# Kernel tuning notes

Hardware: AMD Instinct MI355X
Metric: run time of the kernel (lower is better)

## Reference

```python
import jax, jax.numpy as jnp
import numpy as np

N, C, S = 16, 512, 4096

def setup_inputs() -> dict:
    rng = jax.random.key(0)
    k1, k2, k3 = jax.random.split(rng, 3)
    return {
        "key": jax.random.normal(k1, (N, C, S), dtype=jnp.float32),
        "value": jax.random.normal(k2, (N, C, S), dtype=jnp.float32),
        "query": jax.random.normal(k3, (N, C, S), dtype=jnp.float32),
    }

def reference(key, value, query):
    KC = key.shape[1]
    # query.permute(0,2,1): [N, C, S] -> [N, S, C]
    # sim_map = bmm(key, query^T): [N, C, C], scaled by KC^-0.5
    sim = jnp.einsum("ncs,nds->ncd", key, query) * (KC ** -0.5)
    # softmax over dim=1 (first C axis)
    sim = jax.nn.softmax(sim, axis=1)
    # context = bmm(sim, value): [N, C, C] @ [N, C, S] -> [N, C, S]
    context = jnp.einsum("ncd,nds->ncs", sim, value)
    return context
```

## Files before the change

kernel.cpp:

```cpp
#include <hip/hip_runtime.h>

typedef __bf16 bf16x8 __attribute__((ext_vector_type(8)));
typedef float f32x4 __attribute__((ext_vector_type(4)));
typedef unsigned short u16;
typedef u16 u16x4 __attribute__((ext_vector_type(4)));
typedef u16 u16x8 __attribute__((ext_vector_type(8)));

__device__ __forceinline__ u16 f2bf(float f) {
  unsigned u = __builtin_bit_cast(unsigned, f);
  unsigned r = (u + 0x7fffu + ((u >> 16) & 1u)) >> 16;
  return (u16)r;
}

__device__ __forceinline__ void gld_lds16(const u16* g, u16* l) {
  __builtin_amdgcn_global_load_lds(
      (__attribute__((address_space(1))) void*)(g),
      (__attribute__((address_space(3))) void*)(l), 16, 0, 0);
}

__device__ __forceinline__ f32x4 ntload4(const float* p) {
  return __builtin_nontemporal_load((const f32x4*)p);
}

__global__ __launch_bounds__(256) void k_cvt(const float* __restrict__ K,
                                             const float* __restrict__ Q,
                                             u16* __restrict__ Kb,
                                             u16* __restrict__ Qb) {
  const float* src = blockIdx.y ? Q : K;
  u16* dst = blockIdx.y ? Qb : Kb;
  const size_t i = (size_t)blockIdx.x * 2048 + threadIdx.x * 8;
  f32x4 a = ntload4(src + i);
  f32x4 b = ntload4(src + i + 4);
  u16x8 h;
  h[0] = f2bf(a[0]); h[1] = f2bf(a[1]); h[2] = f2bf(a[2]); h[3] = f2bf(a[3]);
  h[4] = f2bf(b[0]); h[5] = f2bf(b[1]); h[6] = f2bf(b[2]); h[7] = f2bf(b[3]);
  *(u16x8*)(dst + i) = h;
}

__global__ __launch_bounds__(512) void k_mix(const u16* __restrict__ Kb,
                                             const u16* __restrict__ Qb,
                                             float* __restrict__ Lp,
                                             const float* __restrict__ V,
                                             u16* __restrict__ Vt) {
  extern __shared__ char raw[];
  const int bid = blockIdx.x;
  const int t = threadIdx.x;

  if (bid % 5 == 0) {
    u16* sA = (u16*)raw;
    u16* sB = (u16*)(raw + 32768);
    const int sid0 = bid / 5;
    const int sid = (sid0 & 7) * 64 + (sid0 >> 3);
    const int n = sid >> 5;
    const int rem = sid & 31;
    const int kc = rem >> 4;
    const int r2 = rem & 15;
    const int cy = r2 >> 2, dx = r2 & 3;
    const int lane = t & 63, wid = t >> 6;
    const int wr = wid >> 2, wc = wid & 3;
    const float scale = 0.04419417382415922f;

    const u16* Ab = Kb + ((size_t)n * 512 + cy * 128) * 4096 + kc * 2048;
    const u16* Bb = Qb + ((size_t)n * 512 + dx * 128) * 4096 + kc * 2048;
    f32x4 acc[4][2] = {};
    const int srow0 = t >> 3;
    const int scol = ((t & 7) << 3) ^ ((srow0 & 7) << 3);

#define MIX_STAGE(buf, k0)                                                      \
  {                                                                             \
    _Pragma("unroll") for (int q = 0; q < 2; ++q) {                             \
      const int row = q * 64 + srow0;                                           \
      gld_lds16(Ab + (size_t)row * 4096 + (k0) + scol,                          \
                sA + (buf) * 8192 + (q * 512 + (wid << 6)) * 8);                \
      gld_lds16(Bb + (size_t)row * 4096 + (k0) + scol,                          \
                sB + (buf) * 8192 + (q * 512 + (wid << 6)) * 8);                \
    }                                                                           \
  }
#define MIX_COMPUTE(buf)                                                        \
  {                                                                             \
    _Pragma("unroll") for (int ki = 0; ki < 2; ++ki) {                          \
      bf16x8 a[4], b[2];                                                        \
      const int ce = ki * 32 + (lane >> 4) * 8;                                 \
      _Pragma("unroll") for (int mi = 0; mi < 4; ++mi) {                        \
        const int r = wr * 64 + mi * 16 + (lane & 15);                          \
        a[mi] = *(const bf16x8*)&sA[(buf) * 8192 + r * 64 + (ce ^ ((r & 7) << 3))]; \
      }                                                                         \
      _Pragma("unroll") for (int ni = 0; ni < 2; ++ni) {                        \
        const int r = wc * 32 + ni * 16 + (lane & 15);                          \
        b[ni] = *(const bf16x8*)&sB[(buf) * 8192 + r * 64 + (ce ^ ((r & 7) << 3))]; \
      }                                                                         \
      __builtin_amdgcn_s_setprio(1);                                            \
      _Pragma("unroll") for (int mi = 0; mi < 4; ++mi)                          \
        _Pragma("unroll") for (int ni = 0; ni < 2; ++ni)                        \
          acc[mi][ni] = __builtin_amdgcn_mfma_f32_16x16x32_bf16(                \
              a[mi], b[ni], acc[mi][ni], 0, 0, 0);                              \
      __builtin_amdgcn_s_setprio(0);                                            \
    }                                                                           \
  }

    MIX_STAGE(0, 0);
    __syncthreads();
    int cur = 0;
    for (int kt = 0; kt < 31; ++kt) {
      MIX_STAGE(cur ^ 1, (kt + 1) << 6);
      MIX_COMPUTE(cur);
      __syncthreads();
      cur ^= 1;
    }
    MIX_COMPUTE(cur);

    float* Lb = Lp + ((size_t)kc * 16 + n) * 512 * 512;
    const int c0 = cy * 128, d0 = dx * 128;
#pragma unroll
    for (int mi = 0; mi < 4; ++mi)
#pragma unroll
      for (int ni = 0; ni < 2; ++ni) {
        int colo = d0 + wc * 32 + ni * 16 + (lane & 15);
#pragma unroll
        for (int j = 0; j < 4; ++j) {
          int rowo = c0 + wr * 64 + mi * 16 + ((lane >> 4) << 2) + j;
          Lb[(size_t)rowo * 512 + colo] = acc[mi][ni][j] * scale;
        }
      }
#undef MIX_STAGE
#undef MIX_COMPUTE
  } else {
    const int vid = bid - bid / 5 - 1;
    const int sub = t >> 8, tt = t & 255;
    const int tile = vid * 2 + sub;
    const int n = tile >> 8;
    const int r = tile & 255;
    const int d0 = (r >> 6) * 128, s0 = (r & 63) * 64;
    float* lds = (float*)(raw + sub * 34816);
    {
      const int r0 = tt >> 4, c4 = (tt & 15) << 2;
#pragma unroll
      for (int p = 0; p < 8; ++p) {
        const int dr = r0 + p * 16;
        f32x4 v = ntload4(V + ((size_t)n * 512 + d0 + dr) * 4096 + s0 + c4);
        const int sw = ((dr >> 3) & 7) << 2;
        *(f32x4*)(&lds[dr * 68 + (c4 ^ sw)]) = v;
      }
    }
    __syncthreads();
    {
      const int sr0 = tt >> 4, dcol = (tt & 15) << 3;
#pragma unroll
      for (int p2 = 0; p2 < 4; ++p2) {
        const int sr = sr0 + p2 * 16;
        u16x8 h;
#pragma unroll
        for (int j = 0; j < 8; ++j) {
          const int d = dcol + j;
          h[j] = f2bf(lds[d * 68 + (sr ^ (((d >> 3) & 7) << 2))]);
        }
        *(u16x8*)(Vt + ((size_t)n * 4096 + s0 + sr) * 512 + d0 + dcol) = h;
      }
    }
  }
}

template <int KDIV>
__global__ __launch_bounds__(512) void k_stats2(const float* __restrict__ Lp,
                                                u16* __restrict__ E) {
  __shared__ f32x4 redm[16][32];
  __shared__ f32x4 reds[16][32];
  const int n = blockIdx.y;
  const int tx = threadIdx.x & 31, ty = threadIdx.x >> 5;
  const int d0 = blockIdx.x * 128 + tx * 4;
  const size_t CH = (size_t)16 * 512 * 512;
  const float* B = Lp + (size_t)n * 512 * 512 + d0;

  f32x4 m = {-3.0e38f, -3.0e38f, -3.0e38f, -3.0e38f};
  f32x4 s = {0.f, 0.f, 0.f, 0.f};
  for (int c = ty; c < 512; c += 16) {
    f32x4 v = *(const f32x4*)(B + (size_t)c * 512);
#pragma unroll
    for (int q = 1; q < KDIV; ++q) v += *(const f32x4*)(B + q * CH + (size_t)c * 512);
#pragma unroll
    for (int j = 0; j < 4; ++j) {
      float nm = fmaxf(m[j], v[j]);
      s[j] = s[j] * __expf(m[j] - nm) + __expf(v[j] - nm);
      m[j] = nm;
    }
  }
  redm[ty][tx] = m;
  reds[ty][tx] = s;
  __syncthreads();
  f32x4 M = redm[0][tx], S;
#pragma unroll
  for (int q = 1; q < 16; ++q)
#pragma unroll
    for (int j = 0; j < 4; ++j) M[j] = fmaxf(M[j], redm[q][tx][j]);
#pragma unroll
  for (int j = 0; j < 4; ++j) S[j] = 0.f;
#pragma unroll
  for (int q = 0; q < 16; ++q)
#pragma unroll
    for (int j = 0; j < 4; ++j) S[j] += reds[q][tx][j] * __expf(redm[q][tx][j] - M[j]);
  f32x4 si;
#pragma unroll
  for (int j = 0; j < 4; ++j) si[j] = 1.0f / S[j];

  u16* Eb = E + (size_t)n * 512 * 512 + d0;
  for (int c = ty; c < 512; c += 16) {
    f32x4 v = *(const f32x4*)(B + (size_t)c * 512);
#pragma unroll
    for (int q = 1; q < KDIV; ++q) v += *(const f32x4*)(B + q * CH + (size_t)c * 512);
    u16x4 h;
#pragma unroll
    for (int j = 0; j < 4; ++j) h[j] = f2bf(__expf(v[j] - M[j]) * si[j]);
    *(u16x4*)(Eb + (size_t)c * 512) = h;
  }
}

template <int KDIV>
__global__ __launch_bounds__(512) void k_simk(const u16* __restrict__ Kb,
                                              const u16* __restrict__ Qb,
                                              float* __restrict__ Lp) {
  __shared__ u16 sA[2][128 * 64];
  __shared__ u16 sB[2][128 * 64];
  constexpr int NB = 256 * KDIV;
  const int bid = blockIdx.x;
  const int sid = (bid & 7) * (NB / 8) + (bid >> 3);
  constexpr int PER_N = 16 * KDIV;
  const int n = sid / PER_N;
  const int rem = sid % PER_N;
  const int kc = rem >> 4;
  const int r2 = rem & 15;
  const int cy = r2 >> 2, dx = r2 & 3;
  const int t = threadIdx.x, lane = t & 63, wid = t >> 6;
  const int wr = wid >> 2, wc = wid & 3;
  const float scale = 0.04419417382415922f;

  const u16* Ab = Kb + ((size_t)n * 512 + cy * 128) * 4096 + kc * (4096 / KDIV);
  const u16* Bb = Qb + ((size_t)n * 512 + dx * 128) * 4096 + kc * (4096 / KDIV);
  f32x4 acc[4][2] = {};
  const int srow0 = t >> 3;
  const int scol = ((t & 7) << 3) ^ ((srow0 & 7) << 3);

#define SIM_STAGE(buf, k0)                                                      \
  {                                                                             \
    _Pragma("unroll") for (int q = 0; q < 2; ++q) {                             \
      const int row = q * 64 + srow0;                                           \
      gld_lds16(Ab + (size_t)row * 4096 + (k0) + scol,                          \
                &sA[buf][(q * 512 + (wid << 6)) * 8]);                          \
      gld_lds16(Bb + (size_t)row * 4096 + (k0) + scol,                          \
                &sB[buf][(q * 512 + (wid << 6)) * 8]);                          \
    }                                                                           \
  }
#define SIM_COMPUTE(buf)                                                        \
  {                                                                             \
    _Pragma("unroll") for (int ki = 0; ki < 2; ++ki) {                          \
      bf16x8 a[4], b[2];                                                        \
      const int ce = ki * 32 + (lane >> 4) * 8;                                 \
      _Pragma("unroll") for (int mi = 0; mi < 4; ++mi) {                        \
        const int r = wr * 64 + mi * 16 + (lane & 15);                          \
        a[mi] = *(const bf16x8*)&sA[buf][r * 64 + (ce ^ ((r & 7) << 3))];       \
      }                                                                         \
      _Pragma("unroll") for (int ni = 0; ni < 2; ++ni) {                        \
        const int r = wc * 32 + ni * 16 + (lane & 15);                          \
        b[ni] = *(const bf16x8*)&sB[buf][r * 64 + (ce ^ ((r & 7) << 3))];       \
      }                                                                         \
      _Pragma("unroll") for (int mi = 0; mi < 4; ++mi)                          \
        _Pragma("unroll") for (int ni = 0; ni < 2; ++ni)                        \
          acc[mi][ni] = __builtin_amdgcn_mfma_f32_16x16x32_bf16(                \
              a[mi], b[ni], acc[mi][ni], 0, 0, 0);                              \
    }                                                                           \
  }

  constexpr int NSTEP = 64 / KDIV;
  SIM_STAGE(0, 0);
  __syncthreads();
  int cur = 0;
  for (int kt = 0; kt < NSTEP - 1; ++kt) {
    SIM_STAGE(cur ^ 1, (kt + 1) << 6);
    SIM_COMPUTE(cur);
    __syncthreads();
    cur ^= 1;
  }
  SIM_COMPUTE(cur);

  float* Lb = Lp + ((size_t)kc * 16 + n) * 512 * 512;
  const int c0 = cy * 128, d0 = dx * 128;
#pragma unroll
  for (int mi = 0; mi < 4; ++mi)
#pragma unroll
    for (int ni = 0; ni < 2; ++ni) {
      int colo = d0 + wc * 32 + ni * 16 + (lane & 15);
#pragma unroll
      for (int j = 0; j < 4; ++j) {
        int rowo = c0 + wr * 64 + mi * 16 + ((lane >> 4) << 2) + j;
        Lb[(size_t)rowo * 512 + colo] = acc[mi][ni][j] * scale;
      }
    }
#undef SIM_STAGE
#undef SIM_COMPUTE
}

__global__ __launch_bounds__(256) void k_vt(const float* __restrict__ V,
                                            u16* __restrict__ Vt) {
  __shared__ float lds[128 * 68];
  const int n = blockIdx.z, d0 = blockIdx.y * 128, s0 = blockIdx.x * 64;
  const int t = threadIdx.x;
  {
    const int r0 = t >> 4, c4 = (t & 15) << 2;
#pragma unroll
    for (int p = 0; p < 8; ++p) {
      const int dr = r0 + p * 16;
      f32x4 v = ntload4(V + ((size_t)n * 512 + d0 + dr) * 4096 + s0 + c4);
      const int sw = ((dr >> 3) & 7) << 2;
      *(f32x4*)(&lds[dr * 68 + (c4 ^ sw)]) = v;
    }
  }
  __syncthreads();
  {
    const int sr0 = t >> 4, dcol = (t & 15) << 3;
#pragma unroll
    for (int p2 = 0; p2 < 4; ++p2) {
      const int sr = sr0 + p2 * 16;
      u16x8 h;
#pragma unroll
      for (int j = 0; j < 8; ++j) {
        const int d = dcol + j;
        h[j] = f2bf(lds[d * 68 + (sr ^ (((d >> 3) & 7) << 2))]);
      }
      *(u16x8*)(Vt + ((size_t)n * 4096 + s0 + sr) * 512 + d0 + dcol) = h;
    }
  }
}

__global__ __launch_bounds__(512) void k_ctx3(const u16* __restrict__ E,
                                              const u16* __restrict__ Vt,
                                              float* __restrict__ O) {
  __shared__ u16 sA[2][128 * 64];
  __shared__ u16 sB[2][128 * 64];
  const int bid = blockIdx.x;
  const int sid = (bid & 7) * 256 + (bid >> 3);
  const int n = sid >> 7;
  const int rem = sid & 127;
  const int cy = rem >> 5, sx = rem & 31;
  const int t = threadIdx.x, lane = t & 63, wid = t >> 6;
  const int wr = wid >> 2, wc = wid & 3;

  const u16* Ab = E + ((size_t)n * 512 + cy * 128) * 512;
  const u16* Bb = Vt + ((size_t)n * 4096 + sx * 128) * 512;
  const int srow0 = t >> 3;
  const int scol = ((t & 7) << 3) ^ ((srow0 & 7) << 3);
  f32x4 acc[4][2] = {};

#define CTX_STAGE(buf, kd)                                                      \
  {                                                                             \
    _Pragma("unroll") for (int q = 0; q < 2; ++q) {                             \
      const int row = q * 64 + srow0;                                           \
      gld_lds16(Ab + (size_t)row * 512 + (kd) + scol,                           \
                &sA[buf][(q * 512 + (wid << 6)) * 8]);                          \
      gld_lds16(Bb + (size_t)row * 512 + (kd) + scol,                           \
                &sB[buf][(q * 512 + (wid << 6)) * 8]);                          \
    }                                                                           \
  }
#define CTX_COMPUTE(buf)                                                        \
  {                                                                             \
    _Pragma("unroll") for (int ki = 0; ki < 2; ++ki) {                          \
      bf16x8 a[4], b[2];                                                        \
      const int ce = ki * 32 + (lane >> 4) * 8;                                 \
      _Pragma("unroll") for (int mi = 0; mi < 4; ++mi) {                        \
        const int r = wr * 64 + mi * 16 + (lane & 15);                          \
        a[mi] = *(const bf16x8*)&sA[buf][r * 64 + (ce ^ ((r & 7) << 3))];       \
      }                                                                         \
      _Pragma("unroll") for (int ni = 0; ni < 2; ++ni) {                        \
        const int r = wc * 32 + ni * 16 + (lane & 15);                          \
        b[ni] = *(const bf16x8*)&sB[buf][r * 64 + (ce ^ ((r & 7) << 3))];       \
      }                                                                         \
      _Pragma("unroll") for (int mi = 0; mi < 4; ++mi)                          \
        _Pragma("unroll") for (int ni = 0; ni < 2; ++ni)                        \
          acc[mi][ni] = __builtin_amdgcn_mfma_f32_16x16x32_bf16(                \
              a[mi], b[ni], acc[mi][ni], 0, 0, 0);                              \
    }                                                                           \
  }

  CTX_STAGE(0, 0);
  __syncthreads();
  int cur = 0;
  for (int kt = 0; kt < 7; ++kt) {
    CTX_STAGE(cur ^ 1, (kt + 1) << 6);
    CTX_COMPUTE(cur);
    __syncthreads();
    cur ^= 1;
  }
  CTX_COMPUTE(cur);

  float* Ob = O + ((size_t)n * 512 + cy * 128) * 4096 + sx * 128;
#pragma unroll
  for (int mi = 0; mi < 4; ++mi)
#pragma unroll
    for (int ni = 0; ni < 2; ++ni) {
      int colo = wc * 32 + ni * 16 + (lane & 15);
#pragma unroll
      for (int j = 0; j < 4; ++j) {
        int rowo = wr * 64 + mi * 16 + ((lane >> 4) << 2) + j;
        __builtin_nontemporal_store(acc[mi][ni][j], &Ob[(size_t)rowo * 4096 + colo]);
      }
    }
#undef CTX_STAGE
#undef CTX_COMPUTE
}

extern "C" void kernel_launch(void* const* d_in, const int* in_sizes, int n_in,
                              void* d_out, int out_size, void* d_ws, size_t ws_size,
                              hipStream_t stream) {
  const float* Kp = (const float*)d_in[0];
  const float* Vp = (const float*)d_in[1];
  const float* Qp = (const float*)d_in[2];
  float* Op = (float*)d_out;
  char* ws = (char*)d_ws;
  const size_t MB = 1024 * 1024;

  if (ws_size >= 192 * MB) {
    u16* Kb = (u16*)ws;
    u16* Qb = (u16*)(ws + 64 * MB);
    u16* Vt = (u16*)(ws + 128 * MB);
    u16* E  = (u16*)(ws + 64 * MB);
    float* Lp = Op;

    k_cvt<<<dim3(16384, 2), 256, 0, stream>>>(Kp, Qp, Kb, Qb);
    k_mix<<<2560, 512, 69632, stream>>>(Kb, Qb, Lp, Vp, Vt);
    k_stats2<2><<<dim3(4, 16), 512, 0, stream>>>(Lp, E);
    k_ctx3<<<2048, 512, 0, stream>>>(E, Vt, Op);
  } else if (ws_size >= 128 * MB) {
    u16* Kb = (u16*)ws;
    u16* Qb = (u16*)(ws + 64 * MB);
    u16* Vt = (u16*)ws;
    u16* E  = (u16*)(ws + 64 * MB);
    float* Lp = Op;

    k_cvt<<<dim3(16384, 2), 256, 0, stream>>>(Kp, Qp, Kb, Qb);
    k_simk<2><<<512, 512, 0, stream>>>(Kb, Qb, Lp);
    k_stats2<2><<<dim3(4, 16), 512, 0, stream>>>(Lp, E);
    k_vt<<<dim3(64, 4, 16), 256, 0, stream>>>(Vp, Vt);
    k_ctx3<<<2048, 512, 0, stream>>>(E, Vt, Op);
  }
}
```

Measured before the change: 226.8 us.

## Shrink k_mix LDS footprint to single buffer and one V tile per block

```diff
diff --git a/kernel.cpp b/kernel.cpp
--- a/kernel.cpp
+++ b/kernel.cpp
@@ -37,19 +37,19 @@
   *(u16x8*)(dst + i) = h;
 }
 
-__global__ __launch_bounds__(512) void k_mix(const u16* __restrict__ Kb,
-                                             const u16* __restrict__ Qb,
-                                             float* __restrict__ Lp,
-                                             const float* __restrict__ V,
-                                             u16* __restrict__ Vt) {
+__global__ __launch_bounds__(512) void k_mix4(const u16* __restrict__ Kb,
+                                              const u16* __restrict__ Qb,
+                                              float* __restrict__ Lp,
+                                              const float* __restrict__ V,
+                                              u16* __restrict__ Vt) {
   extern __shared__ char raw[];
   const int bid = blockIdx.x;
   const int t = threadIdx.x;
 
-  if (bid % 5 == 0) {
+  if (bid % 9 == 0) {
     u16* sA = (u16*)raw;
-    u16* sB = (u16*)(raw + 32768);
-    const int sid0 = bid / 5;
+    u16* sB = (u16*)(raw + 16384);
+    const int sid0 = bid / 9;
     const int sid = (sid0 & 7) * 64 + (sid0 >> 3);
     const int n = sid >> 5;
     const int rem = sid & 31;
@@ -66,28 +66,28 @@
     const int srow0 = t >> 3;
     const int scol = ((t & 7) << 3) ^ ((srow0 & 7) << 3);
 
-#define MIX_STAGE(buf, k0)                                                      \
+#define MIX_STAGE(k0)                                                           \
   {                                                                             \
     _Pragma("unroll") for (int q = 0; q < 2; ++q) {                             \
       const int row = q * 64 + srow0;                                           \
       gld_lds16(Ab + (size_t)row * 4096 + (k0) + scol,                          \
-                sA + (buf) * 8192 + (q * 512 + (wid << 6)) * 8);                \
+                sA + (q * 512 + (wid << 6)) * 8);                               \
       gld_lds16(Bb + (size_t)row * 4096 + (k0) + scol,                          \
-                sB + (buf) * 8192 + (q * 512 + (wid << 6)) * 8);                \
-    }                                                                           \
-  }
-#define MIX_COMPUTE(buf)                                                        \
+                sB + (q * 512 + (wid << 6)) * 8);                               \
+    }                                                                           \
+  }
+#define MIX_COMPUTE()                                                           \
   {                                                                             \
     _Pragma("unroll") for (int ki = 0; ki < 2; ++ki) {                          \
       bf16x8 a[4], b[2];                                                        \
       const int ce = ki * 32 + (lane >> 4) * 8;                                 \
       _Pragma("unroll") for (int mi = 0; mi < 4; ++mi) {                        \
         const int r = wr * 64 + mi * 16 + (lane & 15);                          \
-        a[mi] = *(const bf16x8*)&sA[(buf) * 8192 + r * 64 + (ce ^ ((r & 7) << 3))]; \
+        a[mi] = *(const bf16x8*)&sA[r * 64 + (ce ^ ((r & 7) << 3))];            \
       }                                                                         \
       _Pragma("unroll") for (int ni = 0; ni < 2; ++ni) {                        \
         const int r = wc * 32 + ni * 16 + (lane & 15);                          \
-        b[ni] = *(const bf16x8*)&sB[(buf) * 8192 + r * 64 + (ce ^ ((r & 7) << 3))]; \
+        b[ni] = *(const bf16x8*)&sB[r * 64 + (ce ^ ((r & 7) << 3))];            \
       }                                                                         \
       __builtin_amdgcn_s_setprio(1);                                            \
       _Pragma("unroll") for (int mi = 0; mi < 4; ++mi)                          \
@@ -98,16 +98,13 @@
     }                                                                           \
   }
 
-    MIX_STAGE(0, 0);
-    __syncthreads();
-    int cur = 0;
-    for (int kt = 0; kt < 31; ++kt) {
-      MIX_STAGE(cur ^ 1, (kt + 1) << 6);
-      MIX_COMPUTE(cur);
+#pragma unroll 1
+    for (int kt = 0; kt < 32; ++kt) {
+      MIX_STAGE(kt << 6);
       __syncthreads();
-      cur ^= 1;
-    }
-    MIX_COMPUTE(cur);
+      MIX_COMPUTE();
+      __syncthreads();
+    }
 
     float* Lb = Lp + ((size_t)kc * 16 + n) * 512 * 512;
     const int c0 = cy * 128, d0 = dx * 128;
@@ -125,18 +122,16 @@
 #undef MIX_STAGE
 #undef MIX_COMPUTE
   } else {
-    const int vid = bid - bid / 5 - 1;
-    const int sub = t >> 8, tt = t & 255;
-    const int tile = vid * 2 + sub;
-    const int n = tile >> 8;
-    const int r = tile & 255;
+    const int vid = bid - bid / 9 - 1;
+    const int n = vid >> 8;
+    const int r = vid & 255;
     const int d0 = (r >> 6) * 128, s0 = (r & 63) * 64;
-    float* lds = (float*)(raw + sub * 34816);
+    float* lds = (float*)raw;
     {
-      const int r0 = tt >> 4, c4 = (tt & 15) << 2;
-#pragma unroll
-      for (int p = 0; p < 8; ++p) {
-        const int dr = r0 + p * 16;
+      const int r0 = t >> 4, c4 = (t & 15) << 2;
+#pragma unroll
+      for (int p = 0; p < 4; ++p) {
+        const int dr = r0 + p * 32;
         f32x4 v = ntload4(V + ((size_t)n * 512 + d0 + dr) * 4096 + s0 + c4);
         const int sw = ((dr >> 3) & 7) << 2;
         *(f32x4*)(&lds[dr * 68 + (c4 ^ sw)]) = v;
@@ -144,10 +139,10 @@
     }
     __syncthreads();
     {
-      const int sr0 = tt >> 4, dcol = (tt & 15) << 3;
-#pragma unroll
-      for (int p2 = 0; p2 < 4; ++p2) {
-        const int sr = sr0 + p2 * 16;
+      const int sr0 = t >> 4, dcol = (t & 15) << 3;
+#pragma unroll
+      for (int p2 = 0; p2 < 2; ++p2) {
+        const int sr = sr0 + p2 * 32;
         u16x8 h;
 #pragma unroll
         for (int j = 0; j < 8; ++j) {
@@ -424,7 +419,7 @@
     float* Lp = Op;
 
     k_cvt<<<dim3(16384, 2), 256, 0, stream>>>(Kp, Qp, Kb, Qb);
-    k_mix<<<2560, 512, 69632, stream>>>(Kb, Qb, Lp, Vp, Vt);
+    k_mix4<<<4608, 512, 34816, stream>>>(Kb, Qb, Lp, Vp, Vt);
     k_stats2<2><<<dim3(4, 16), 512, 0, stream>>>(Lp, E);
     k_ctx3<<<2048, 512, 0, stream>>>(E, Vt, Op);
   } else if (ws_size >= 128 * MB) {
```

Measured after the change: 229.3 us. Within noise of the previous version (+1.1%).
